# Optimization experiments

Hardware: AMD Instinct MI355X
Metric: run time of the kernel (lower is better)

## Reference

```python
import jax, jax.numpy as jnp
import numpy as np

NUM_STEPS = 32
BETA = 0.9
THRESHOLD = 1.0   # LIF firing threshold
LAT_THR = 0.01    # snntorch spikegen.latency default threshold
EPS = 1e-7        # snntorch epsilon
SLOPE = 25.0      # fast_sigmoid surrogate slope
ENC_THR = 0.75    # SpikeEncoder latency_threshold

B, S, F_IN = 512, 64, 128
HIDDEN = [256, 256, 128]


def spike_fn(u):
    # Heaviside forward; surrogate grad handled in fwdbwd module. Forward-only here.
    return (u > 0).astype(u.dtype)


def latency_encode(x, num_steps):
    """SpikeEncoder('latency') -> snntorch.spikegen.latency, normalize=True, linear=False."""
    # gate small values
    x = jnp.where(x < ENC_THR, jnp.zeros_like(x), x)
    # per-channel min-max normalization over the sequence dim (dim=1)
    x_min = jnp.min(x, axis=1, keepdims=True)
    x_max = jnp.max(x, axis=1, keepdims=True)
    xn = (x - x_min) / (x_max - x_min + 1e-8)
    # logarithmic latency code (tau=1, first_spike_time=0, normalize=True)
    d = jnp.clip(xn, LAT_THR + EPS, None)
    t = jnp.log(d / (d - LAT_THR))
    t_max = np.log((LAT_THR + EPS) / EPS)  # spike time of smallest intensity
    t = t * (num_steps - 1) / np.float32(t_max)
    t_idx = jnp.clip(jnp.round(t), 0, num_steps - 1).astype(jnp.int32)  # (B,S,F)
    # one-hot over time -> (T, B, S, F), matches spikegen scatter
    steps = jnp.arange(num_steps, dtype=jnp.int32).reshape(-1, 1, 1, 1)
    return (steps == t_idx[None]).astype(jnp.float32)


def snn_block(x, W, b, beta, thr):
    """Linear over all timesteps, then LIF (reset-by-subtraction) via scan.
    x: (T, B, in) -> spk: (T, B, hidden)"""
    cur = jnp.einsum('tbi,hi->tbh', x, W) + b

    def step(mem, c):
        # snntorch Leaky: reset computed from previous mem (detached)
        reset = jax.lax.stop_gradient((mem - thr > 0).astype(mem.dtype))
        mem = beta * mem + c - reset * thr
        spk = spike_fn(mem - thr)
        return mem, spk

    mem0 = jnp.zeros(cur.shape[1:], cur.dtype)
    _, spk = jax.lax.scan(step, cur[0] * 0 + mem0, cur)
    return spk


def setup_inputs() -> dict:
    key = jax.random.key(0)
    ks = jax.random.split(key, 7)
    x = jax.random.normal(ks[0], (B, S, F_IN), dtype=jnp.float32)
    sizes = [F_IN] + HIDDEN
    params = {}
    for i in range(3):
        fan_in = sizes[i]
        bound = 1.0 / np.sqrt(fan_in)
        params[f'W{i+1}'] = jax.random.uniform(ks[2 * i + 1], (sizes[i + 1], fan_in),
                                               minval=-bound, maxval=bound, dtype=jnp.float32)
        params[f'b{i+1}'] = jax.random.uniform(ks[2 * i + 2], (sizes[i + 1],),
                                               minval=-bound, maxval=bound, dtype=jnp.float32)
    return {'x': x, **params}


def reference(x, W1, b1, W2, b2, W3, b3):
    spikes = latency_encode(x, NUM_STEPS)        # (T, B, S, F)
    spikes = spikes.mean(axis=2)                 # (T, B, F)
    spikes = snn_block(spikes, W1, b1, BETA, THRESHOLD)
    spikes = snn_block(spikes, W2, b2, BETA, THRESHOLD)
    spikes = snn_block(spikes, W3, b3, BETA, THRESHOLD)
    return spikes                                # (T, B, hidden_sizes[-1])
```

## Files before the change

### kernel.cpp

```cpp
#include <hip/hip_runtime.h>
#include <cstddef>

#define T_STEPS 32
#define B_SZ    512
#define S_SZ    64
#define F_INPUT 128
#define H1      256
#define H2      256
#define H3      128

typedef _Float16 half_t;
typedef __attribute__((ext_vector_type(8))) _Float16 half8;
typedef __attribute__((ext_vector_type(4))) float   float4v;

__device__ inline void split_store_sw(float w, half_t* out, int n, int k, int kchunks) {
    half_t hi = (half_t)w;
    float hif = (float)hi;
    if (fabsf(hif) < 6.103515625e-05f) { hi = (half_t)0.0f; hif = 0.0f; }
    half_t lo = (half_t)((w - hif) * 4096.0f);
    int n_tile = n >> 4, lr = n & 15;
    int k_chunk = k >> 5, kin = k & 31, quad = kin >> 3, j = kin & 7;
    size_t base = (size_t)(n_tile * kchunks + k_chunk) * 1024;
    size_t off  = base + (size_t)((quad << 4) + lr) * 8 + j;
    out[off]       = hi;
    out[off + 512] = lo;
}

__global__ __launch_bounds__(256)
void prep_w_kernel(const float* __restrict__ W1, const float* __restrict__ W2,
                   const float* __restrict__ W3,
                   half_t* __restrict__ ws1, half_t* __restrict__ ws2,
                   half_t* __restrict__ ws3) {
    int e = blockIdx.x * blockDim.x + threadIdx.x;
    if (e < H1 * F_INPUT) {
        split_store_sw(W1[e], ws1, e / F_INPUT, e % F_INPUT, F_INPUT / 32);
    } else if (e < H1 * F_INPUT + H2 * H1) {
        int i = e - H1 * F_INPUT;
        split_store_sw(W2[i], ws2, i / H1, i % H1, H1 / 32);
    } else {
        int i = e - H1 * F_INPUT - H2 * H1;
        split_store_sw(W3[i], ws3, i / H2, i % H2, H2 / 32);
    }
}

#define CUR_STRIDE 260
#define AS_STRIDE  136
#define SPK_STRIDE 264
#define SMEM_CUR   0
#define SMEM_AS    33280
#define SMEM_SPK   33280
#define SMEM_TOTAL 50176

template<int KCHUNKS, int NT, int ASTRIDE>
__device__ __forceinline__ void gemm_phase(const half_t* __restrict__ Wsw,
                                           const float*  __restrict__ bias,
                                           const half_t* __restrict__ Als,
                                           float* __restrict__ curT,
                                           int wave, int lane) {
    const int quad = lane >> 4, lr = lane & 15;
    float4v acc_h[2][NT], acc_l[2][NT];
#pragma unroll
    for (int mt = 0; mt < 2; ++mt)
#pragma unroll
        for (int nt = 0; nt < NT; ++nt) {
            acc_h[mt][nt] = (float4v){0.0f, 0.0f, 0.0f, 0.0f};
            acc_l[mt][nt] = (float4v){0.0f, 0.0f, 0.0f, 0.0f};
        }

    half8 wh[NT], wl[NT];
#pragma unroll
    for (int nt = 0; nt < NT; ++nt) {
        const half_t* p = Wsw + ((size_t)(wave * NT + nt) * KCHUNKS) * 1024 + lane * 8;
        wh[nt] = *(const half8*)(p);
        wl[nt] = *(const half8*)(p + 512);
    }

#pragma unroll
    for (int c = 0; c < KCHUNKS; ++c) {
        half8 a0 = *(const half8*)(Als + lr * ASTRIDE        + c * 32 + quad * 8);
        half8 a1 = *(const half8*)(Als + (16 + lr) * ASTRIDE + c * 32 + quad * 8);
        half8 nwh[NT], nwl[NT];
        if (c + 1 < KCHUNKS) {
#pragma unroll
            for (int nt = 0; nt < NT; ++nt) {
                const half_t* p =
                    Wsw + ((size_t)(wave * NT + nt) * KCHUNKS + c + 1) * 1024 + lane * 8;
                nwh[nt] = *(const half8*)(p);
                nwl[nt] = *(const half8*)(p + 512);
            }
        }
#pragma unroll
        for (int nt = 0; nt < NT; ++nt) {
            acc_h[0][nt] = __builtin_amdgcn_mfma_f32_16x16x32_f16(a0, wh[nt], acc_h[0][nt], 0, 0, 0);
            acc_h[1][nt] = __builtin_amdgcn_mfma_f32_16x16x32_f16(a1, wh[nt], acc_h[1][nt], 0, 0, 0);
            acc_l[0][nt] = __builtin_amdgcn_mfma_f32_16x16x32_f16(a0, wl[nt], acc_l[0][nt], 0, 0, 0);
            acc_l[1][nt] = __builtin_amdgcn_mfma_f32_16x16x32_f16(a1, wl[nt], acc_l[1][nt], 0, 0, 0);
        }
#pragma unroll
        for (int nt = 0; nt < NT; ++nt) { wh[nt] = nwh[nt]; wl[nt] = nwl[nt]; }
    }

#pragma unroll
    for (int nt = 0; nt < NT; ++nt) {
        int col = wave * NT * 16 + nt * 16 + lr;
        float bj = bias[col];
#pragma unroll
        for (int mt = 0; mt < 2; ++mt) {
            int rbase = mt * 16 + quad * 4;
#pragma unroll
            for (int r = 0; r < 4; ++r) {
                float v = acc_h[mt][nt][r] + 2.44140625e-04f * acc_l[mt][nt][r];
                curT[(rbase + r) * CUR_STRIDE + col] = v + bj;
            }
        }
    }
}

__global__ __launch_bounds__(512, 4)
void snn_mega_kernel(const float* __restrict__ x,
                     const half_t* __restrict__ ws1, const float* __restrict__ b1,
                     const half_t* __restrict__ ws2, const float* __restrict__ b2,
                     const half_t* __restrict__ ws3, const float* __restrict__ b3,
                     float* __restrict__ out) {
    __shared__ __align__(16) char smem[SMEM_TOTAL];
    float*  curT = (float*) (smem + SMEM_CUR);
    half_t* As   = (half_t*)(smem + SMEM_AS);
    half_t* spk  = (half_t*)(smem + SMEM_SPK);

    const int tid  = threadIdx.x;
    const int b    = blockIdx.x;
    const int wave = tid >> 6;
    const int lane = tid & 63;

    const int f  = tid & 127;
    const int sh = (tid >> 7) & 1;
    const float* xp = x + (size_t)b * (S_SZ * F_INPUT) + (size_t)sh * 32 * F_INPUT + f;
    float* scratch = curT;

    float v[32];
    if (tid < 256) {
#pragma unroll
        for (int s = 0; s < 32; ++s) {
            float val = xp[(size_t)s * F_INPUT];
            v[s] = (val < 0.75f) ? 0.0f : val;
        }
        float mn = 1e30f, mx = -1e30f;
#pragma unroll
        for (int s = 0; s < 32; ++s) {
            mn = fminf(mn, v[s]);
            mx = fmaxf(mx, v[s]);
        }
        scratch[sh * 128 + f]       = mn;
        scratch[256 + sh * 128 + f] = mx;
    }
    __syncthreads();
    float fmn = fminf(scratch[f], scratch[128 + f]);
    float fmx = fmaxf(scratch[256 + f], scratch[384 + f]);
    __syncthreads();

    unsigned* histu = (unsigned*)scratch;
    if (tid < 256) {
#pragma unroll
        for (int t = 0; t < T_STEPS; ++t) histu[sh * 4096 + t * 128 + f] = 0u;
        const float denom = fmx - fmn + 1e-8f;
#pragma unroll
        for (int s = 0; s < 32; ++s) {
            float g = v[s];
            float xn = (g - fmn) / denom;
            float d  = fmaxf(xn, 0.0100001f);
            float tt = logf(d / (d - 0.01f));
            tt = tt * 31.0f;
            tt = tt / 11.512935464920229f;
            float tr = rintf(tt);
            tr = fminf(fmaxf(tr, 0.0f), 31.0f);
            atomicAdd(&histu[sh * 4096 + (int)tr * 128 + f], 1u);
        }
    }
    __syncthreads();

#pragma unroll
    for (int i = 0; i < 8; ++i) {
        int idx = tid + i * 512;
        int t = idx >> 7, ff = idx & 127;
        float cnt = (float)(histu[t * 128 + ff] + histu[4096 + t * 128 + ff]);
        As[t * AS_STRIDE + ff] = (half_t)(cnt * 0.015625f);
    }
    __syncthreads();

    gemm_phase<F_INPUT / 32, 2, AS_STRIDE>(ws1, b1, As, curT, wave, lane);
    __syncthreads();
    if (tid < 256) {
#pragma clang fp contract(off)
        const int h = tid;
        float mem = 0.0f;
#pragma unroll
        for (int t = 0; t < T_STEPS; ++t) {
            float c = curT[t * CUR_STRIDE + h];
            float reset = (mem - 1.0f > 0.0f) ? 1.0f : 0.0f;
            float p = 0.9f * mem;
            p = p + c;
            mem = p - reset;
            spk[t * SPK_STRIDE + h] = (half_t)((mem - 1.0f > 0.0f) ? 1.0f : 0.0f);
        }
    }
    __syncthreads();

    gemm_phase<H1 / 32, 2, SPK_STRIDE>(ws2, b2, spk, curT, wave, lane);
    __syncthreads();
    if (tid < 256) {
#pragma clang fp contract(off)
        const int h = tid;
        float mem = 0.0f;
#pragma unroll
        for (int t = 0; t < T_STEPS; ++t) {
            float c = curT[t * CUR_STRIDE + h];
            float reset = (mem - 1.0f > 0.0f) ? 1.0f : 0.0f;
            float p = 0.9f * mem;
            p = p + c;
            mem = p - reset;
            spk[t * SPK_STRIDE + h] = (half_t)((mem - 1.0f > 0.0f) ? 1.0f : 0.0f);
        }
    }
    __syncthreads();

    gemm_phase<H2 / 32, 1, SPK_STRIDE>(ws3, b3, spk, curT, wave, lane);
    __syncthreads();
    if (tid < H3) {
#pragma clang fp contract(off)
        const int h = tid;
        float mem = 0.0f;
#pragma unroll
        for (int t = 0; t < T_STEPS; ++t) {
            float c = curT[t * CUR_STRIDE + h];
            float reset = (mem - 1.0f > 0.0f) ? 1.0f : 0.0f;
            float p = 0.9f * mem;
            p = p + c;
            mem = p - reset;
            out[((size_t)t * B_SZ + b) * H3 + h] = (mem - 1.0f > 0.0f) ? 1.0f : 0.0f;
        }
    }
}

extern "C" void kernel_launch(void* const* d_in, const int* in_sizes, int n_in,
                              void* d_out, int out_size, void* d_ws, size_t ws_size,
                              hipStream_t stream) {
    const float* x  = (const float*)d_in[0];
    const float* W1 = (const float*)d_in[1];
    const float* b1 = (const float*)d_in[2];
    const float* W2 = (const float*)d_in[3];
    const float* b2 = (const float*)d_in[4];
    const float* W3 = (const float*)d_in[5];
    const float* b3 = (const float*)d_in[6];
    float* out = (float*)d_out;

    char* ws = (char*)d_ws;
    half_t* ws1 = (half_t*)ws;
    half_t* ws2 = (half_t*)(ws + 128 * 1024);
    half_t* ws3 = (half_t*)(ws + 384 * 1024);

    prep_w_kernel<<<(H1 * F_INPUT + H2 * H1 + H3 * H2) / 256, 256, 0, stream>>>(
        W1, W2, W3, ws1, ws2, ws3);

    snn_mega_kernel<<<B_SZ, 512, 0, stream>>>(x, ws1, b1, ws2, b2, ws3, b3, out);
}
```

Baseline: 97.13 us.

## Fuse weight preparation into main kernel with grid-wide flag barrier

Removes the separate weight split/swizzle kernel. Each of the 512 blocks now converts 256 weight elements while it computes its encoder min/max, then publishes a sentinel flag. Every block spins on all 512 flags before its first GEMM, which removes one kernel launch and its serialization gap. This relies on all blocks being co-resident. The flags are also never reset, so on later calls a block can see stale sentinels and read weights that are still being rewritten.

```diff
diff --git a/kernel.cpp b/kernel.cpp
--- a/kernel.cpp
+++ b/kernel.cpp
@@ -12,6 +12,8 @@
 typedef _Float16 half_t;
 typedef __attribute__((ext_vector_type(8))) _Float16 half8;
 typedef __attribute__((ext_vector_type(4))) float   float4v;
+
+#define PREP_SENT 0x1A2B3C4Du
 
 __device__ inline void split_store_sw(float w, half_t* out, int n, int k, int kchunks) {
     half_t hi = (half_t)w;
@@ -26,23 +28,6 @@
     out[off + 512] = lo;
 }
 
-__global__ __launch_bounds__(256)
-void prep_w_kernel(const float* __restrict__ W1, const float* __restrict__ W2,
-                   const float* __restrict__ W3,
-                   half_t* __restrict__ ws1, half_t* __restrict__ ws2,
-                   half_t* __restrict__ ws3) {
-    int e = blockIdx.x * blockDim.x + threadIdx.x;
-    if (e < H1 * F_INPUT) {
-        split_store_sw(W1[e], ws1, e / F_INPUT, e % F_INPUT, F_INPUT / 32);
-    } else if (e < H1 * F_INPUT + H2 * H1) {
-        int i = e - H1 * F_INPUT;
-        split_store_sw(W2[i], ws2, i / H1, i % H1, H1 / 32);
-    } else {
-        int i = e - H1 * F_INPUT - H2 * H1;
-        split_store_sw(W3[i], ws3, i / H2, i % H2, H2 / 32);
-    }
-}
-
 #define CUR_STRIDE 260
 #define AS_STRIDE  136
 #define SPK_STRIDE 264
@@ -118,9 +103,12 @@
 
 __global__ __launch_bounds__(512, 4)
 void snn_mega_kernel(const float* __restrict__ x,
-                     const half_t* __restrict__ ws1, const float* __restrict__ b1,
-                     const half_t* __restrict__ ws2, const float* __restrict__ b2,
-                     const half_t* __restrict__ ws3, const float* __restrict__ b3,
+                     const float* __restrict__ W1raw, const float* __restrict__ W2raw,
+                     const float* __restrict__ W3raw,
+                     half_t* __restrict__ ws1, const float* __restrict__ b1,
+                     half_t* __restrict__ ws2, const float* __restrict__ b2,
+                     half_t* __restrict__ ws3, const float* __restrict__ b3,
+                     unsigned* __restrict__ flags,
                      float* __restrict__ out) {
     __shared__ __align__(16) char smem[SMEM_TOTAL];
     float*  curT = (float*) (smem + SMEM_CUR);
@@ -132,6 +120,14 @@
     const int wave = tid >> 6;
     const int lane = tid & 63;
 
+    float wprep = 0.0f;
+    if (tid < 256) {
+        int e = b * 256 + tid;
+        wprep = (b < 128) ? W1raw[e]
+              : (b < 384) ? W2raw[e - H1 * F_INPUT]
+                          : W3raw[e - H1 * F_INPUT - H2 * H1];
+    }
+
     const int f  = tid & 127;
     const int sh = (tid >> 7) & 1;
     const float* xp = x + (size_t)b * (S_SZ * F_INPUT) + (size_t)sh * 32 * F_INPUT + f;
@@ -152,8 +148,23 @@
         }
         scratch[sh * 128 + f]       = mn;
         scratch[256 + sh * 128 + f] = mx;
-    }
-    __syncthreads();
+
+        int e = b * 256 + tid;
+        if (b < 128) {
+            split_store_sw(wprep, ws1, e / F_INPUT, e % F_INPUT, F_INPUT / 32);
+        } else if (b < 384) {
+            int i = e - H1 * F_INPUT;
+            split_store_sw(wprep, ws2, i / H1, i % H1, H1 / 32);
+        } else {
+            int i = e - H1 * F_INPUT - H2 * H1;
+            split_store_sw(wprep, ws3, i / H2, i % H2, H2 / 32);
+        }
+    }
+    __syncthreads();
+    if (tid == 0)
+        __hip_atomic_store(&flags[b], PREP_SENT, __ATOMIC_RELEASE,
+                           __HIP_MEMORY_SCOPE_AGENT);
+
     float fmn = fminf(scratch[f], scratch[128 + f]);
     float fmx = fmaxf(scratch[256 + f], scratch[384 + f]);
     __syncthreads();
@@ -186,6 +197,12 @@
         As[t * AS_STRIDE + ff] = (half_t)(cnt * 0.015625f);
     }
     __syncthreads();
+
+    while (__hip_atomic_load(&flags[tid], __ATOMIC_RELAXED,
+                             __HIP_MEMORY_SCOPE_AGENT) != PREP_SENT)
+        __builtin_amdgcn_s_sleep(2);
+    __syncthreads();
+    __builtin_amdgcn_fence(__ATOMIC_ACQUIRE, "agent");
 
     gemm_phase<F_INPUT / 32, 2, AS_STRIDE>(ws1, b1, As, curT, wave, lane);
     __syncthreads();
@@ -254,12 +271,12 @@
     float* out = (float*)d_out;
 
     char* ws = (char*)d_ws;
-    half_t* ws1 = (half_t*)ws;
-    half_t* ws2 = (half_t*)(ws + 128 * 1024);
-    half_t* ws3 = (half_t*)(ws + 384 * 1024);
-
-    prep_w_kernel<<<(H1 * F_INPUT + H2 * H1 + H3 * H2) / 256, 256, 0, stream>>>(
-        W1, W2, W3, ws1, ws2, ws3);
-
-    snn_mega_kernel<<<B_SZ, 512, 0, stream>>>(x, ws1, b1, ws2, b2, ws3, b3, out);
-}
+    half_t*   ws1   = (half_t*)ws;
+    half_t*   ws2   = (half_t*)(ws + 128 * 1024);
+    half_t*   ws3   = (half_t*)(ws + 384 * 1024);
+    unsigned* flags = (unsigned*)(ws + 512 * 1024);
+
+    snn_mega_kernel<<<B_SZ, 512, 0, stream>>>(x, W1, W2, W3,
+                                              ws1, b1, ws2, b2, ws3, b3,
+                                              flags, out);
+}
```

After: 131.2 us. 1.35x slower.
